# Optimization experiments

Hardware: AMD Instinct MI355X
Metric: run time of the kernel (lower is better)

Reference implementation:

```python
import jax, jax.numpy as jnp
import numpy as np

NF, NX, GROUP_SIZE = 8192, 2048, 64
N_GROUPS = NX // GROUP_SIZE  # pad = 0 since NX % GROUP_SIZE == 0


def setup_inputs() -> dict:
    key = jax.random.key(0)
    k1, k2, k3, k4, k5 = jax.random.split(key, 5)
    x = jax.random.normal(k1, (4, 2048, NX), dtype=jnp.float32)
    packed = jax.random.randint(k2, (NF, NX // 2), 0, 256, dtype=jnp.int32)
    scales = jax.random.uniform(k3, (NF, N_GROUPS), dtype=jnp.float32)
    zeros = jax.random.randint(k4, (NF, N_GROUPS), 0, 16, dtype=jnp.int32)
    bias = jax.random.normal(k5, (NF,), dtype=jnp.float32)
    return {"x": x, "packed": packed, "scales": scales, "zeros": zeros, "bias": bias}


def _dequantize(packed, scales, zeros):
    # packed: [nf, nx//2] bytes, two int4 nibbles per byte (low nibble first)
    low = packed & 15
    high = (packed >> 4) & 15
    # interleave: q[:, 0::2] = low, q[:, 1::2] = high
    q = jnp.stack([low, high], axis=-1).reshape(NF, NX).astype(jnp.float32)
    q = q.reshape(NF, N_GROUPS, GROUP_SIZE)
    W = (q - zeros.astype(jnp.float32)[:, :, None]) * scales[:, :, None]
    return W.reshape(NF, NX)  # [nf, nx]


def reference(x, packed, scales, zeros, bias):
    W = _dequantize(packed, scales, zeros).astype(x.dtype)  # [nf, nx]
    size_out = x.shape[:-1] + (NF,)
    out = jnp.matmul(x.reshape(-1, NX), W.T) + bias  # addmm
    return out.reshape(size_out)
```

## Files before the change

### kernel.cpp

```cpp
#include <hip/hip_runtime.h>
#include <stdint.h>

#define NF 8192
#define NX 2048
#define MROWS 8192
#define NGROUPS 32
#define NSTEP 64

typedef unsigned short u16;
typedef __bf16 bf16x8 __attribute__((ext_vector_type(8)));
typedef float f32x4 __attribute__((ext_vector_type(4)));

#define AS1 __attribute__((address_space(1)))
#define AS3 __attribute__((address_space(3)))

__device__ __forceinline__ void glds16(const void* g, void* l) {
    __builtin_amdgcn_global_load_lds((AS1 void*)(uintptr_t)g,
                                     (AS3 void*)(uintptr_t)l, 16, 0, 0);
}

__device__ __forceinline__ u16 f2bf(float f) {
    unsigned u = __float_as_uint(f);
    return (u16)((u + 0x7FFFu + ((u >> 16) & 1u)) >> 16);
}

__global__ void dequant_kernel(const int* __restrict__ packed,
                               const float* __restrict__ scales,
                               const int* __restrict__ zeros,
                               uint32_t* __restrict__ W2) {
    int tid = blockIdx.x * blockDim.x + threadIdx.x;
    int f = tid >> 10;
    int i = tid & 1023;
    int g = f * NGROUPS + (i >> 5);
    int p = packed[tid];
    float s = scales[g];
    float z = (float)zeros[g];
    float w0 = ((float)(p & 15) - z) * s;
    float w1 = ((float)((p >> 4) & 15) - z) * s;
    W2[tid] = (uint32_t)f2bf(w0) | ((uint32_t)f2bf(w1) << 16);
}

__global__ void cvt_kernel(const float4* __restrict__ x, ushort4* __restrict__ y) {
    int i = blockIdx.x * blockDim.x + threadIdx.x;
    float4 v = x[i];
    ushort4 o;
    o.x = f2bf(v.x); o.y = f2bf(v.y); o.z = f2bf(v.z); o.w = f2bf(v.w);
    y[i] = o;
}


#define BAR    __builtin_amdgcn_s_barrier()
#define LGKM0  asm volatile("s_waitcnt lgkmcnt(0)" ::: "memory")
#define VMCNT6 asm volatile("s_waitcnt vmcnt(6)" ::: "memory")
#define VMCNT0 asm volatile("s_waitcnt vmcnt(0)" ::: "memory")
#define FENCE  __builtin_amdgcn_sched_barrier(0)

#define LD8(off) (*(const bf16x8*)(smem + (off)))

#define STAGE6(REG, S) do { \
    const char* _sa = srcA + (size_t)(S) * 64; \
    const char* _sb = srcB + (size_t)(S) * 64; \
    glds16(_sa,          smem + (REG) + t16); \
    glds16(_sa + 262144, smem + (REG) + 4096  + t16); \
    glds16(_sa + 524288, smem + (REG) + 8192  + t16); \
    glds16(_sa + 786432, smem + (REG) + 12288 + t16); \
    glds16(_sb,          smem + (REG) + 16384 + t16); \
    glds16(_sb + 262144, smem + (REG) + 20480 + t16); \
} while (0)

__global__ __launch_bounds__(256, 2)
void gemm_kernel(const u16* __restrict__ A, const u16* __restrict__ B,
                 const float* __restrict__ bias, float* __restrict__ C) {
    __shared__ __align__(16) char smem[73728];

    const int t = threadIdx.x;

    const int bid = blockIdx.x;
    const int xcd = bid & 7;
    const int local = bid >> 3;
    const int super = local >> 7;
    const int r = local & 127;
    const int by = xcd * 4 + super * 2 + (r & 1);
    const int bx = r >> 1;
    const int rowA0 = by * 256;
    const int rowB0 = bx * 128;

    const int t16 = t * 16;
    const int kslot = (t & 3) ^ ((t >> 3) & 3);
    const char* srcA = (const char*)A + (size_t)(rowA0 + (t >> 2)) * 4096 + kslot * 16;
    const char* srcB = (const char*)B + (size_t)(rowB0 + (t >> 2)) * 4096 + kslot * 16;

    const int lane = t & 63;
    const int wv = t >> 6;
    const int wm = wv >> 1;
    const int wn = wv & 1;
    const int l15 = lane & 15;
    const int quad = lane >> 4;
    const int uX = ((((l15 >> 1) & 3) ^ quad)) << 4;
    const int aOff = (wm * 128 + l15) * 64 + uX;
    const int bOff = 16384 + (wn * 64 + l15) * 64 + uX;

    f32x4 acc[8][4];
#pragma unroll
    for (int i = 0; i < 8; ++i)
#pragma unroll
        for (int j = 0; j < 4; ++j) acc[i][j] = {0.f, 0.f, 0.f, 0.f};

    bf16x8 a[8], b[4];

    STAGE6(0,     0);
    STAGE6(24576, 1);
    VMCNT6;

    int regC = 0, regN = 24576, regT = 49152;

#pragma unroll 1
    for (int s = 0; s < NSTEP; ++s) {
        FENCE; BAR; FENCE;
#pragma unroll
        for (int i = 0; i < 8; ++i) a[i] = LD8(regC + aOff + i * 1024);
#pragma unroll
        for (int j = 0; j < 4; ++j) b[j] = LD8(regC + bOff + j * 1024);
        if (s + 2 < NSTEP) STAGE6(regT, s + 2);
        FENCE; LGKM0; FENCE;
        __builtin_amdgcn_s_setprio(1);
#pragma unroll
        for (int i = 0; i < 8; ++i)
#pragma unroll
            for (int j = 0; j < 4; ++j)
                acc[i][j] = __builtin_amdgcn_mfma_f32_16x16x32_bf16(a[i], b[j], acc[i][j], 0, 0, 0);
        __builtin_amdgcn_s_setprio(0);
        FENCE;
        if (s + 2 < NSTEP) VMCNT6;
        else if (s + 1 < NSTEP) VMCNT0;

        const int tmp = regC; regC = regN; regN = regT; regT = tmp;
    }

    const int col0 = rowB0 + wn * 64 + l15;
    const int row0 = rowA0 + wm * 128 + quad * 4;
    float bj[4];
#pragma unroll
    for (int j = 0; j < 4; ++j) bj[j] = bias[col0 + j * 16];
#pragma unroll
    for (int i = 0; i < 8; ++i) {
#pragma unroll
        for (int e = 0; e < 4; ++e) {
            float* crow = C + (size_t)(row0 + i * 16 + e) * NF;
#pragma unroll
            for (int j = 0; j < 4; ++j)
                __builtin_nontemporal_store(acc[i][j][e] + bj[j], crow + col0 + j * 16);
        }
    }
}

extern "C" void kernel_launch(void* const* d_in, const int* in_sizes, int n_in,
                              void* d_out, int out_size, void* d_ws, size_t ws_size,
                              hipStream_t stream) {
    const float* x      = (const float*)d_in[0];
    const int* packed   = (const int*)d_in[1];
    const float* scales = (const float*)d_in[2];
    const int* zeros    = (const int*)d_in[3];
    const float* bias   = (const float*)d_in[4];
    float* out = (float*)d_out;

    u16* Wq = (u16*)d_ws;
    u16* Xb = Wq + (size_t)NF * NX;

    dequant_kernel<<<(NF * (NX / 2)) / 256, 256, 0, stream>>>(packed, scales, zeros, (uint32_t*)Wq);
    cvt_kernel<<<(MROWS * NX / 4) / 256, 256, 0, stream>>>((const float4*)x, (ushort4*)Xb);

    gemm_kernel<<<dim3((MROWS / 256) * (NF / 128)), 256, 0, stream>>>(Xb, Wq, bias, out);
}
```

Before: 306.3 us.

## Enlarge GEMM tile to 256x256 with 4-stage LDS ring and register double-buffering

The GEMM block grows from 256x128 with 256 threads to 256x256 with 512 threads (8 waves), which raises data reuse per loaded byte. Shared memory becomes a 4-slot ring of 32 KB stages, so global-to-LDS copies are issued three steps ahead. LDS-to-register fragments are double-buffered: the next step's reads are issued before the current step's MFMAs and waited on with a partial lgkmcnt, so LDS latency overlaps compute. The cost is 128 KB of LDS per block, which likely limits residency to one block per CU, plus higher register pressure from the doubled fragments.

```diff
diff --git a/kernel.cpp b/kernel.cpp
--- a/kernel.cpp
+++ b/kernel.cpp
@@ -6,6 +6,7 @@
 #define MROWS 8192
 #define NGROUPS 32
 #define NSTEP 64
+#define RSTRIDE 32768
 
 typedef unsigned short u16;
 typedef __bf16 bf16x8 __attribute__((ext_vector_type(8)));
@@ -50,40 +51,66 @@
 
 
 #define BAR    __builtin_amdgcn_s_barrier()
+#define LGKM12 asm volatile("s_waitcnt lgkmcnt(12)" ::: "memory")
 #define LGKM0  asm volatile("s_waitcnt lgkmcnt(0)" ::: "memory")
-#define VMCNT6 asm volatile("s_waitcnt vmcnt(6)" ::: "memory")
+#define VMCNT4 asm volatile("s_waitcnt vmcnt(4)" ::: "memory")
 #define VMCNT0 asm volatile("s_waitcnt vmcnt(0)" ::: "memory")
 #define FENCE  __builtin_amdgcn_sched_barrier(0)
 
 #define LD8(off) (*(const bf16x8*)(smem + (off)))
 
-#define STAGE6(REG, S) do { \
+#define MFMA(d, va, vb) d = __builtin_amdgcn_mfma_f32_16x16x32_bf16(va, vb, d, 0, 0, 0)
+
+#define STAGE4(REG, S) do { \
     const char* _sa = srcA + (size_t)(S) * 64; \
     const char* _sb = srcB + (size_t)(S) * 64; \
     glds16(_sa,          smem + (REG) + t16); \
-    glds16(_sa + 262144, smem + (REG) + 4096  + t16); \
     glds16(_sa + 524288, smem + (REG) + 8192  + t16); \
-    glds16(_sa + 786432, smem + (REG) + 12288 + t16); \
     glds16(_sb,          smem + (REG) + 16384 + t16); \
-    glds16(_sb + 262144, smem + (REG) + 20480 + t16); \
+    glds16(_sb + 524288, smem + (REG) + 24576 + t16); \
 } while (0)
 
-__global__ __launch_bounds__(256, 2)
+#define STEP(S, CA, CB, NA, NB) do { \
+    FENCE; BAR; FENCE; \
+    if ((S) + 1 < NSTEP) { \
+        const int rN = (((S) + 1) & 3) * RSTRIDE; \
+        _Pragma("unroll") \
+        for (int i_ = 0; i_ < 8; ++i_) NA[i_] = LD8(rN + aOff + i_ * 1024); \
+        _Pragma("unroll") \
+        for (int j_ = 0; j_ < 4; ++j_) NB[j_] = LD8(rN + bOff + j_ * 1024); \
+    } \
+    FENCE; \
+    if ((S) + 3 < NSTEP) STAGE4((((S) + 3) & 3) * RSTRIDE, (S) + 3); \
+    FENCE; \
+    if ((S) + 1 < NSTEP) { LGKM12; } else { LGKM0; } \
+    FENCE; \
+    __builtin_amdgcn_s_setprio(1); \
+    _Pragma("unroll") \
+    for (int i_ = 0; i_ < 8; ++i_) \
+        _Pragma("unroll") \
+        for (int j_ = 0; j_ < 4; ++j_) MFMA(acc[i_][j_], CA[i_], CB[j_]); \
+    __builtin_amdgcn_s_setprio(0); \
+    FENCE; \
+    if ((S) <= NSTEP - 4) { VMCNT4; } \
+    else if ((S) == NSTEP - 3) { VMCNT0; } \
+} while (0)
+
+__global__ __launch_bounds__(512, 2)
 void gemm_kernel(const u16* __restrict__ A, const u16* __restrict__ B,
                  const float* __restrict__ bias, float* __restrict__ C) {
-    __shared__ __align__(16) char smem[73728];
+    __shared__ __align__(16) char smem[131072];
 
     const int t = threadIdx.x;
 
     const int bid = blockIdx.x;
     const int xcd = bid & 7;
     const int local = bid >> 3;
-    const int super = local >> 7;
-    const int r = local & 127;
+    const int super = local >> 6;
+    const int r = local & 63;
     const int by = xcd * 4 + super * 2 + (r & 1);
     const int bx = r >> 1;
     const int rowA0 = by * 256;
-    const int rowB0 = bx * 128;
+    const int rowB0 = bx * 256;
 
     const int t16 = t * 16;
     const int kslot = (t & 3) ^ ((t >> 3) & 3);
@@ -92,11 +119,11 @@
 
     const int lane = t & 63;
     const int wv = t >> 6;
-    const int wm = wv >> 1;
-    const int wn = wv & 1;
+    const int wm = wv >> 2;
+    const int wn = wv & 3;
     const int l15 = lane & 15;
     const int quad = lane >> 4;
-    const int uX = ((((l15 >> 1) & 3) ^ quad)) << 4;
+    const int uX = (quad ^ ((l15 >> 1) & 3)) << 4;
     const int aOff = (wm * 128 + l15) * 64 + uX;
     const int bOff = 16384 + (wn * 64 + l15) * 64 + uX;
 
@@ -106,35 +133,22 @@
 #pragma unroll
         for (int j = 0; j < 4; ++j) acc[i][j] = {0.f, 0.f, 0.f, 0.f};
 
-    bf16x8 a[8], b[4];
+    bf16x8 aA[8], bA[4], aB[8], bB[4];
 
-    STAGE6(0,     0);
-    STAGE6(24576, 1);
-    VMCNT6;
-
-    int regC = 0, regN = 24576, regT = 49152;
+    STAGE4(0,           0);
+    STAGE4(RSTRIDE,     1);
+    STAGE4(2 * RSTRIDE, 2);
+    VMCNT4;
+    BAR;
+#pragma unroll
+    for (int i = 0; i < 8; ++i) aA[i] = LD8(aOff + i * 1024);
+#pragma unroll
+    for (int j = 0; j < 4; ++j) bA[j] = LD8(bOff + j * 1024);
 
 #pragma unroll 1
-    for (int s = 0; s < NSTEP; ++s) {
-        FENCE; BAR; FENCE;
-#pragma unroll
-        for (int i = 0; i < 8; ++i) a[i] = LD8(regC + aOff + i * 1024);
-#pragma unroll
-        for (int j = 0; j < 4; ++j) b[j] = LD8(regC + bOff + j * 1024);
-        if (s + 2 < NSTEP) STAGE6(regT, s + 2);
-        FENCE; LGKM0; FENCE;
-        __builtin_amdgcn_s_setprio(1);
-#pragma unroll
-        for (int i = 0; i < 8; ++i)
-#pragma unroll
-            for (int j = 0; j < 4; ++j)
-                acc[i][j] = __builtin_amdgcn_mfma_f32_16x16x32_bf16(a[i], b[j], acc[i][j], 0, 0, 0);
-        __builtin_amdgcn_s_setprio(0);
-        FENCE;
-        if (s + 2 < NSTEP) VMCNT6;
-        else if (s + 1 < NSTEP) VMCNT0;
-
-        const int tmp = regC; regC = regN; regN = regT; regT = tmp;
+    for (int s = 0; s < NSTEP; s += 2) {
+        STEP(s,     aA, bA, aB, bB);
+        STEP(s + 1, aB, bB, aA, bA);
     }
 
     const int col0 = rowB0 + wn * 64 + l15;
@@ -170,5 +184,5 @@
     dequant_kernel<<<(NF * (NX / 2)) / 256, 256, 0, stream>>>(packed, scales, zeros, (uint32_t*)Wq);
     cvt_kernel<<<(MROWS * NX / 4) / 256, 256, 0, stream>>>((const float4*)x, (ushort4*)Xb);
 
-    gemm_kernel<<<dim3((MROWS / 256) * (NF / 128)), 256, 0, stream>>>(Xb, Wq, bias, out);
+    gemm_kernel<<<dim3((MROWS / 256) * (NF / 256)), 512, 0, stream>>>(Xb, Wq, bias, out);
 }
```

Measured after the change: 302.2 us. Within noise of the previous version (-1.3%).
